# Optimization experiments

Measured on AMD Instinct MI355X. Metric: run time of the kernel, lower is better.

## Reference

```python
import jax, jax.numpy as jnp
import numpy as np

N_NODES = 100000
N_EDGES = 3200000
NUM_FEATURES = 128
DIM = 10
NUM_GRAPHS = 64


def setup_inputs() -> dict:
    key = jax.random.key(0)
    k1, k2, k3, k4, k5, k6, k7 = jax.random.split(key, 7)
    features = jax.random.normal(k1, (N_NODES, NUM_FEATURES), dtype=jnp.float32)
    src = jax.random.randint(k2, (N_EDGES,), 0, N_NODES, dtype=jnp.int64)
    dst = jax.random.randint(k3, (N_EDGES,), 0, N_NODES, dtype=jnp.int64)
    graph_ids = jnp.sort(jax.random.randint(k4, (N_NODES,), 0, NUM_GRAPHS, dtype=jnp.int64))
    # GraphConv weights (no bias), glorot-ish scaling
    W1 = jax.random.normal(k5, (NUM_FEATURES, DIM), dtype=jnp.float32) / np.sqrt(NUM_FEATURES)
    W2 = jax.random.normal(k6, (DIM, DIM), dtype=jnp.float32) / np.sqrt(DIM)
    W3 = jax.random.normal(k7, (DIM, 1), dtype=jnp.float32) / np.sqrt(DIM)
    return {"features": features, "W1": W1, "W2": W2, "W3": W3,
            "src": src, "dst": dst, "graph_ids": graph_ids}


def _sum_aggregate(h, src, dst, n_nodes):
    # message = h[src], reduce-sum at dst (norm='none' GraphConv aggregation)
    return jax.ops.segment_sum(h[src], dst, num_segments=n_nodes)


def reference(features, W1, W2, W3, src, dst, graph_ids):
    n = features.shape[0]
    # conv1: in_feats(128) > out_feats(10) -> weight first, then aggregate
    h = features @ W1                          # [N, DIM]
    h = _sum_aggregate(h, src, dst, n)         # [N, DIM]
    h = jax.nn.relu(h)
    # conv2: in_feats == out_feats -> aggregate first, then weight
    h = _sum_aggregate(h, src, dst, n) @ W2    # [N, DIM]
    # dgl.mean_nodes: per-graph mean pooling over nodes
    sums = jax.ops.segment_sum(h, graph_ids, num_segments=NUM_GRAPHS)           # [G, DIM]
    cnt = jax.ops.segment_sum(jnp.ones((n, 1), h.dtype), graph_ids, num_segments=NUM_GRAPHS)
    pooled = sums / jnp.maximum(cnt, 1.0)      # [G, DIM]
    return jax.nn.sigmoid(pooled @ W3)         # [G, 1]
```

## Files before the change

kernel.cpp:

```cpp
#include <hip/hip_runtime.h>
#include <hip/hip_fp16.h>

#define N_NODES 100000
#define N_EDGES 3200000
#define NUM_FEATURES 128
#define DIM 10
#define NUM_GRAPHS 64

#define BSHIFT 8
#define BSIZE (1 << BSHIFT)
#define NB ((N_NODES + BSIZE - 1) / BSIZE)
#define CHUNKS 2
#define PCHUNKS 4
#define EPB 12500
#define PLACE_BLOCKS 256
#define GEMM_BLOCKS 6250
#define BOUND_BLOCKS 196
#define TILE (BSIZE * DIM)
#define CAP 4608
#define CAPB 16384
#define NCHUNK (NB * CHUNKS)
#define NCHUNK2 (NB * PCHUNKS)
#define ACC_STRIDE 11

__global__ __launch_bounds__(512) void k_front(const float* __restrict__ feat,
                                               const float* __restrict__ W1,
                                               __half* __restrict__ h1,
                                               const int* __restrict__ gids,
                                               int* __restrict__ bound,
                                               const int* __restrict__ src,
                                               const int* __restrict__ dst,
                                               int* __restrict__ cnt,
                                               int* __restrict__ pk) {
    __shared__ int hd[NB];
    __shared__ int cb[NB];

    if (blockIdx.x < PLACE_BLOCKS) {
        int base0 = blockIdx.x * EPB;
        for (int t = threadIdx.x; t < NB; t += 512) hd[t] = 0;
        __syncthreads();

        {
            int i = threadIdx.x;
            for (; i + 1536 < EPB; i += 2048) {
                int d0 = dst[base0 + i],        d1 = dst[base0 + i + 512];
                int d2 = dst[base0 + i + 1024], d3 = dst[base0 + i + 1536];
                atomicAdd(&hd[d0 >> BSHIFT], 1);
                atomicAdd(&hd[d1 >> BSHIFT], 1);
                atomicAdd(&hd[d2 >> BSHIFT], 1);
                atomicAdd(&hd[d3 >> BSHIFT], 1);
            }
            for (; i < EPB; i += 512) {
                int d = dst[base0 + i];
                atomicAdd(&hd[d >> BSHIFT], 1);
            }
        }
        __syncthreads();

        for (int t = threadIdx.x; t < NB; t += 512) {
            int c = hd[t];
            int o = c ? atomicAdd(&cnt[t], c) : 0;
            cb[t] = t * CAPB + o;
        }
        __syncthreads();

        {
            int i = threadIdx.x;
            for (; i + 1536 < EPB; i += 2048) {
                int d0 = dst[base0 + i],        d1 = dst[base0 + i + 512];
                int d2 = dst[base0 + i + 1024], d3 = dst[base0 + i + 1536];
                int s0 = src[base0 + i],        s1 = src[base0 + i + 512];
                int s2 = src[base0 + i + 1024], s3 = src[base0 + i + 1536];
                int q0 = atomicAdd(&cb[d0 >> BSHIFT], 1);
                int q1 = atomicAdd(&cb[d1 >> BSHIFT], 1);
                int q2 = atomicAdd(&cb[d2 >> BSHIFT], 1);
                int q3 = atomicAdd(&cb[d3 >> BSHIFT], 1);
                if (q0 < ((d0 >> BSHIFT) + 1) * CAPB) pk[q0] = ((d0 & (BSIZE - 1)) << 17) | s0;
                if (q1 < ((d1 >> BSHIFT) + 1) * CAPB) pk[q1] = ((d1 & (BSIZE - 1)) << 17) | s1;
                if (q2 < ((d2 >> BSHIFT) + 1) * CAPB) pk[q2] = ((d2 & (BSIZE - 1)) << 17) | s2;
                if (q3 < ((d3 >> BSHIFT) + 1) * CAPB) pk[q3] = ((d3 & (BSIZE - 1)) << 17) | s3;
            }
            for (; i < EPB; i += 512) {
                int d = dst[base0 + i];
                int s = src[base0 + i];
                int q = atomicAdd(&cb[d >> BSHIFT], 1);
                if (q < ((d >> BSHIFT) + 1) * CAPB) pk[q] = ((d & (BSIZE - 1)) << 17) | s;
            }
        }
        return;
    }

    int bb = blockIdx.x - PLACE_BLOCKS;

    int nb2 = bb * 512 + threadIdx.x;
    if (bb < BOUND_BLOCKS && nb2 < N_NODES) {
        int g  = gids[nb2];
        int gp = nb2 ? gids[nb2 - 1] : -1;
        for (int v = gp + 1; v <= g; ++v) bound[v] = nb2;
        if (nb2 == N_NODES - 1)
            for (int v = g + 1; v <= NUM_GRAPHS; ++v) bound[v] = N_NODES;
    }

    int gid  = bb * 512 + threadIdx.x;
    int node = gid >> 5;
    int lane = gid & 31;
    if (node >= N_NODES) return;

    float w[4][DIM];
#pragma unroll
    for (int j = 0; j < 4; ++j)
#pragma unroll
        for (int k = 0; k < DIM; ++k)
            w[j][k] = W1[(lane * 4 + j) * DIM + k];

    const float4 f = *reinterpret_cast<const float4*>(feat + (size_t)node * NUM_FEATURES + lane * 4);
    float fv[4] = {f.x, f.y, f.z, f.w};

    float acc[DIM];
#pragma unroll
    for (int k = 0; k < DIM; ++k) acc[k] = 0.f;
#pragma unroll
    for (int j = 0; j < 4; ++j)
#pragma unroll
        for (int k = 0; k < DIM; ++k)
            acc[k] += fv[j] * w[j][k];

#pragma unroll
    for (int off = 16; off > 0; off >>= 1)
#pragma unroll
        for (int k = 0; k < DIM; ++k)
            acc[k] += __shfl_xor(acc[k], off);

    if (lane == 0) {
        __half2* o = (__half2*)h1;
#pragma unroll
        for (int j = 0; j < 5; ++j)
            o[(size_t)node * 5 + j] = __floats2half2_rn(acc[2 * j], acc[2 * j + 1]);
    }
}

__global__ __launch_bounds__(512) void k_spmm1(const __half* __restrict__ h,
                                               const int* __restrict__ cnt,
                                               const int* __restrict__ pk,
                                               float* __restrict__ part) {
    __shared__ int eh[CAP];
    __shared__ int srt[CAP];
    __shared__ int hist[BSIZE];
    __shared__ int cur[BSIZE];

    int b     = blockIdx.x / CHUNKS;
    int chunk = blockIdx.x % CHUNKS;
    int s0  = b * CAPB;
    int len = cnt[b];
    int c0  = s0 + (len * chunk) / CHUNKS;
    int c1  = s0 + (len * (chunk + 1)) / CHUNKS;
    int n   = c1 - c0;
    int nc  = min(n, CAP);

    for (int t = threadIdx.x; t < BSIZE; t += 512) hist[t] = 0;
    __syncthreads();

    {
        int i = threadIdx.x;
        for (; i + 1536 < nc; i += 2048) {
            int p0 = pk[c0 + i],        p1 = pk[c0 + i + 512];
            int p2 = pk[c0 + i + 1024], p3 = pk[c0 + i + 1536];
            eh[i] = p0; eh[i + 512] = p1; eh[i + 1024] = p2; eh[i + 1536] = p3;
            atomicAdd(&hist[p0 >> 17], 1);
            atomicAdd(&hist[p1 >> 17], 1);
            atomicAdd(&hist[p2 >> 17], 1);
            atomicAdd(&hist[p3 >> 17], 1);
        }
        for (; i < nc; i += 512) {
            int p = pk[c0 + i];
            eh[i] = p;
            atomicAdd(&hist[p >> 17], 1);
        }
    }
    __syncthreads();

    if (threadIdx.x < 64) {
        int l = threadIdx.x;
        int carry = 0;
#pragma unroll
        for (int j = 0; j < 4; ++j) {
            int x = hist[j * 64 + l];
            int v = x;
#pragma unroll
            for (int off = 1; off < 64; off <<= 1) {
                int t2 = __shfl_up(v, off);
                if (l >= off) v += t2;
            }
            cur[j * 64 + l] = carry + v - x;
            carry += __shfl(v, 63);
        }
    }
    __syncthreads();

    for (int i = threadIdx.x; i < nc; i += 512) {
        int p = eh[i];
        int pos = atomicAdd(&cur[p >> 17], 1);
        srt[pos] = p;
    }
    __syncthreads();

    int wave = threadIdx.x >> 6;
    int lane = threadIdx.x & 63;
    int slot = lane / 5;
    int l    = lane - slot * 5;
    float* pb = part + (size_t)blockIdx.x * TILE;
    const __half2* h2 = (const __half2*)h;

    if (slot < 12) {
        int g = wave * 12 + slot;
        for (int loc = g; loc < BSIZE; loc += 96) {
            int e0 = loc ? cur[loc - 1] : 0;
            int e1 = cur[loc];
            float ax0 = 0.f, ay0 = 0.f, ax1 = 0.f, ay1 = 0.f;
            float ax2 = 0.f, ay2 = 0.f, ax3 = 0.f, ay3 = 0.f;
            int e = e0;
            for (; e + 7 < e1; e += 8) {
                float2 v0 = __half22float2(h2[(size_t)(srt[e]     & 0x1FFFF) * 5 + l]);
                float2 v1 = __half22float2(h2[(size_t)(srt[e + 1] & 0x1FFFF) * 5 + l]);
                float2 v2 = __half22float2(h2[(size_t)(srt[e + 2] & 0x1FFFF) * 5 + l]);
                float2 v3 = __half22float2(h2[(size_t)(srt[e + 3] & 0x1FFFF) * 5 + l]);
                float2 v4 = __half22float2(h2[(size_t)(srt[e + 4] & 0x1FFFF) * 5 + l]);
                float2 v5 = __half22float2(h2[(size_t)(srt[e + 5] & 0x1FFFF) * 5 + l]);
                float2 v6 = __half22float2(h2[(size_t)(srt[e + 6] & 0x1FFFF) * 5 + l]);
                float2 v7 = __half22float2(h2[(size_t)(srt[e + 7] & 0x1FFFF) * 5 + l]);
                ax0 += v0.x + v4.x; ay0 += v0.y + v4.y;
                ax1 += v1.x + v5.x; ay1 += v1.y + v5.y;
                ax2 += v2.x + v6.x; ay2 += v2.y + v6.y;
                ax3 += v3.x + v7.x; ay3 += v3.y + v7.y;
            }
            for (; e < e1; ++e) {
                float2 v = __half22float2(h2[(size_t)(srt[e] & 0x1FFFF) * 5 + l]);
                ax0 += v.x; ay0 += v.y;
            }
            pb[loc * DIM + 2 * l]     = (ax0 + ax1) + (ax2 + ax3);
            pb[loc * DIM + 2 * l + 1] = (ay0 + ay1) + (ay2 + ay3);
        }
    }
    __syncthreads();

    for (int i = CAP + threadIdx.x; i < n; i += 512) {
        int p = pk[c0 + i];
        int loc = p >> 17, s = p & 0x1FFFF;
#pragma unroll
        for (int j = 0; j < 5; ++j) {
            float2 v = __half22float2(h2[(size_t)s * 5 + j]);
            atomicAdd(&pb[loc * DIM + 2 * j], v.x);
            atomicAdd(&pb[loc * DIM + 2 * j + 1], v.y);
        }
    }
}

__global__ __launch_bounds__(256) void k_merge_relu(const float* __restrict__ part,
                                                    __half* __restrict__ r) {
    int b     = blockIdx.x;
    int nbase = b << BSHIFT;
    const float* p0 = part + (size_t)(b * CHUNKS) * TILE;
    __half2* r2 = (__half2*)r;
    for (int t = threadIdx.x; t < TILE / 2; t += 256) {
        float sx = 0.f, sy = 0.f;
#pragma unroll
        for (int c = 0; c < CHUNKS; ++c) {
            float2 v = ((const float2*)(p0 + (size_t)c * TILE))[t];
            sx += v.x; sy += v.y;
        }
        int ebase = nbase * DIM + 2 * t;
        if (ebase < N_NODES * DIM)
            r2[(size_t)nbase * 5 + t] = __floats2half2_rn(fmaxf(sx, 0.f), fmaxf(sy, 0.f));
    }
}

__global__ __launch_bounds__(512) void k_pass2(const __half* __restrict__ r,
                                               const int* __restrict__ cnt,
                                               const int* __restrict__ pk,
                                               const int* __restrict__ bound,
                                               float* __restrict__ sums) {
    __shared__ float acc[NUM_GRAPHS * ACC_STRIDE];

    int b     = blockIdx.x / PCHUNKS;
    int chunk = blockIdx.x % PCHUNKS;
    int nbase = b << BSHIFT;
    int nlast = min(nbase + BSIZE - 1, N_NODES - 1);

    int glo = 0, ghx = NUM_GRAPHS - 1;
#pragma unroll
    for (int it = 0; it < 6; ++it) {
        int mid = (glo + ghx + 1) >> 1;
        if (bound[mid] <= nbase) glo = mid; else ghx = mid - 1;
    }
    int lo2 = 0, hi2 = NUM_GRAPHS - 1;
#pragma unroll
    for (int it = 0; it < 6; ++it) {
        int mid = (lo2 + hi2 + 1) >> 1;
        if (bound[mid] <= nlast) lo2 = mid; else hi2 = mid - 1;
    }
    int ghi  = lo2;
    int span = ghi - glo;

    for (int t = threadIdx.x; t < (span + 1) * DIM; t += 512)
        acc[(glo + t / DIM) * ACC_STRIDE + t % DIM] = 0.f;
    __syncthreads();

    int s0  = b * CAPB;
    int len = cnt[b];
    int c0  = s0 + (len * chunk) / PCHUNKS;
    int c1  = s0 + (len * (chunk + 1)) / PCHUNKS;

    int wave = threadIdx.x >> 6;
    int lane = threadIdx.x & 63;
    int slot = lane / 5;
    int l    = lane - slot * 5;
    const __half2* r2 = (const __half2*)r;

    if (slot < 12) {
        const int STR = 96;
        int q = wave * 12 + slot;
        int e = c0 + q;
        if (span <= 1) {
            int gA  = glo;
            int gB  = (span == 1) ? glo + 1 : glo;
            int cut = (span == 1) ? (bound[glo + 1] - nbase) : BSIZE;
            float axA = 0.f, ayA = 0.f, axB = 0.f, ayB = 0.f;
            for (; e + 7 * STR < c1; e += 8 * STR) {
                int p[8];
#pragma unroll
                for (int u = 0; u < 8; ++u) p[u] = pk[e + u * STR];
                float2 v[8];
#pragma unroll
                for (int u = 0; u < 8; ++u)
                    v[u] = __half22float2(r2[(size_t)(p[u] & 0x1FFFF) * 5 + l]);
#pragma unroll
                for (int u = 0; u < 8; ++u) {
                    bool a = (p[u] >> 17) < cut;
                    axA += a ? v[u].x : 0.f;  ayA += a ? v[u].y : 0.f;
                    axB += a ? 0.f : v[u].x;  ayB += a ? 0.f : v[u].y;
                }
            }
            for (; e < c1; e += STR) {
                int p = pk[e];
                float2 v = __half22float2(r2[(size_t)(p & 0x1FFFF) * 5 + l]);
                bool a = (p >> 17) < cut;
                axA += a ? v.x : 0.f;  ayA += a ? v.y : 0.f;
                axB += a ? 0.f : v.x;  ayB += a ? 0.f : v.y;
            }
            atomicAdd(&acc[gA * ACC_STRIDE + 2 * l], axA);
            atomicAdd(&acc[gA * ACC_STRIDE + 2 * l + 1], ayA);
            if (span == 1) {
                atomicAdd(&acc[gB * ACC_STRIDE + 2 * l], axB);
                atomicAdd(&acc[gB * ACC_STRIDE + 2 * l + 1], ayB);
            }
        } else {
            for (; e < c1; e += STR) {
                int p   = pk[e];
                int loc = p >> 17;
                float2 v = __half22float2(r2[(size_t)(p & 0x1FFFF) * 5 + l]);
                int g = glo;
                for (int gg = glo + 1; gg <= ghi; ++gg)
                    g += (loc >= bound[gg] - nbase) ? 1 : 0;
                atomicAdd(&acc[g * ACC_STRIDE + 2 * l], v.x);
                atomicAdd(&acc[g * ACC_STRIDE + 2 * l + 1], v.y);
            }
        }
    }
    __syncthreads();

    for (int t = threadIdx.x; t < (span + 1) * DIM; t += 512) {
        int g = glo + t / DIM;
        float v = acc[g * ACC_STRIDE + t % DIM];
        if (v != 0.f) atomicAdd(&sums[g * DIM + t % DIM], v);
    }
}

__global__ void k_final(const float* __restrict__ sums, const int* __restrict__ bound,
                        const float* __restrict__ W2, const float* __restrict__ W3,
                        float* __restrict__ out) {
    int g = threadIdx.x;
    if (g >= NUM_GRAPHS) return;
    float c = fmaxf((float)(bound[g + 1] - bound[g]), 1.f);
    float p[DIM];
#pragma unroll
    for (int k = 0; k < DIM; ++k) p[k] = sums[g * DIM + k] / c;
    float z = 0.f;
#pragma unroll
    for (int j = 0; j < DIM; ++j) {
        float t = 0.f;
#pragma unroll
        for (int k = 0; k < DIM; ++k) t += p[k] * W2[k * DIM + j];
        z += t * W3[j];
    }
    out[g] = 1.f / (1.f + expf(-z));
}

extern "C" void kernel_launch(void* const* d_in, const int* in_sizes, int n_in,
                              void* d_out, int out_size, void* d_ws, size_t ws_size,
                              hipStream_t stream) {
    const float* feat = (const float*)d_in[0];
    const float* W1   = (const float*)d_in[1];
    const float* W2   = (const float*)d_in[2];
    const float* W3   = (const float*)d_in[3];
    const int*   src  = (const int*)d_in[4];
    const int*   dst  = (const int*)d_in[5];
    const int*   gids = (const int*)d_in[6];
    float*       out  = (float*)d_out;

    char* ws = (char*)d_ws;
    __half* h1    = (__half*)(ws);
    int*    pk    = (int*)(ws + 2000000);
    __half* r     = (__half*)(ws + 27624576);
    float*  part  = (float*)(ws + 29624576);
    int*    cnt   = (int*)(ws + 37632256);
    float*  sums  = (float*)(ws + 37633824);
    int*    bound = (int*)(ws + 37636384);

    hipMemsetAsync(ws + 37632256, 0, 4128, stream);

    k_front<<<PLACE_BLOCKS + GEMM_BLOCKS, 512, 0, stream>>>(feat, W1, h1, gids, bound,
                                                            src, dst, cnt, pk);
    k_spmm1     <<<NCHUNK, 512, 0, stream>>>(h1, cnt, pk, part);
    k_merge_relu<<<NB, 256, 0, stream>>>(part, r);
    k_pass2     <<<NCHUNK2, 512, 0, stream>>>(r, cnt, pk, bound, sums);

    k_final<<<1, 64, 0, stream>>>(sums, bound, W2, W3, out);
}
```

Before: 215.5 us.

## Fuse merge-relu and final into last-block epilogues, DPP reduce, more place blocks

Removes the separate merge/relu and final kernels by having the last-arriving chunk block (tracked by an atomic counter) do the merge+ReLU, and the last pass2 block compute the pooled output. It also replaces the shuffle reduction in the GEMM with DPP row-rotate adds, drops the shared staging buffer in spmm1 by rereading pk from global memory, and doubles the number of placement blocks. Together these cut launch overhead and shared memory use, at the cost of extra global reads and serialized tail work in the elected blocks.

New measurement: 373.3 us. +73.2%, slower.

```diff
diff --git a/kernel.cpp b/kernel.cpp
--- a/kernel.cpp
+++ b/kernel.cpp
@@ -12,8 +12,8 @@
 #define NB ((N_NODES + BSIZE - 1) / BSIZE)
 #define CHUNKS 2
 #define PCHUNKS 4
-#define EPB 12500
-#define PLACE_BLOCKS 256
+#define EPB 6250
+#define PLACE_BLOCKS 512
 #define GEMM_BLOCKS 6250
 #define BOUND_BLOCKS 196
 #define TILE (BSIZE * DIM)
@@ -22,6 +22,10 @@
 #define NCHUNK (NB * CHUNKS)
 #define NCHUNK2 (NB * PCHUNKS)
 #define ACC_STRIDE 11
+
+#define DPP_ROR_ADD(v, n)                                                        \
+    (v) += __int_as_float(__builtin_amdgcn_update_dpp(                           \
+        0, __float_as_int(v), 0x120 | (n), 0xF, 0xF, false))
 
 __global__ __launch_bounds__(512) void k_front(const float* __restrict__ feat,
                                                const float* __restrict__ W1,
@@ -126,10 +130,14 @@
             acc[k] += fv[j] * w[j][k];
 
 #pragma unroll
-    for (int off = 16; off > 0; off >>= 1)
-#pragma unroll
-        for (int k = 0; k < DIM; ++k)
-            acc[k] += __shfl_xor(acc[k], off);
+    for (int k = 0; k < DIM; ++k) {
+        float v = acc[k];
+        DPP_ROR_ADD(v, 1);
+        DPP_ROR_ADD(v, 2);
+        DPP_ROR_ADD(v, 4);
+        DPP_ROR_ADD(v, 8);
+        acc[k] = v + __shfl_xor(v, 16);
+    }
 
     if (lane == 0) {
         __half2* o = (__half2*)h1;
@@ -142,11 +150,13 @@
 __global__ __launch_bounds__(512) void k_spmm1(const __half* __restrict__ h,
                                                const int* __restrict__ cnt,
                                                const int* __restrict__ pk,
-                                               float* __restrict__ part) {
-    __shared__ int eh[CAP];
+                                               float* __restrict__ part,
+                                               int* __restrict__ done,
+                                               __half* __restrict__ r) {
     __shared__ int srt[CAP];
     __shared__ int hist[BSIZE];
     __shared__ int cur[BSIZE];
+    __shared__ int elect;
 
     int b     = blockIdx.x / CHUNKS;
     int chunk = blockIdx.x % CHUNKS;
@@ -165,17 +175,13 @@
         for (; i + 1536 < nc; i += 2048) {
             int p0 = pk[c0 + i],        p1 = pk[c0 + i + 512];
             int p2 = pk[c0 + i + 1024], p3 = pk[c0 + i + 1536];
-            eh[i] = p0; eh[i + 512] = p1; eh[i + 1024] = p2; eh[i + 1536] = p3;
             atomicAdd(&hist[p0 >> 17], 1);
             atomicAdd(&hist[p1 >> 17], 1);
             atomicAdd(&hist[p2 >> 17], 1);
             atomicAdd(&hist[p3 >> 17], 1);
         }
-        for (; i < nc; i += 512) {
-            int p = pk[c0 + i];
-            eh[i] = p;
-            atomicAdd(&hist[p >> 17], 1);
-        }
+        for (; i < nc; i += 512)
+            atomicAdd(&hist[pk[c0 + i] >> 17], 1);
     }
     __syncthreads();
 
@@ -197,10 +203,20 @@
     }
     __syncthreads();
 
-    for (int i = threadIdx.x; i < nc; i += 512) {
-        int p = eh[i];
-        int pos = atomicAdd(&cur[p >> 17], 1);
-        srt[pos] = p;
+    {
+        int i = threadIdx.x;
+        for (; i + 1536 < nc; i += 2048) {
+            int p0 = pk[c0 + i],        p1 = pk[c0 + i + 512];
+            int p2 = pk[c0 + i + 1024], p3 = pk[c0 + i + 1536];
+            srt[atomicAdd(&cur[p0 >> 17], 1)] = p0;
+            srt[atomicAdd(&cur[p1 >> 17], 1)] = p1;
+            srt[atomicAdd(&cur[p2 >> 17], 1)] = p2;
+            srt[atomicAdd(&cur[p3 >> 17], 1)] = p3;
+        }
+        for (; i < nc; i += 512) {
+            int p = pk[c0 + i];
+            srt[atomicAdd(&cur[p >> 17], 1)] = p;
+        }
     }
     __syncthreads();
 
@@ -253,24 +269,29 @@
             atomicAdd(&pb[loc * DIM + 2 * j + 1], v.y);
         }
     }
-}
-
-__global__ __launch_bounds__(256) void k_merge_relu(const float* __restrict__ part,
-                                                    __half* __restrict__ r) {
-    int b     = blockIdx.x;
-    int nbase = b << BSHIFT;
-    const float* p0 = part + (size_t)(b * CHUNKS) * TILE;
-    __half2* r2 = (__half2*)r;
-    for (int t = threadIdx.x; t < TILE / 2; t += 256) {
-        float sx = 0.f, sy = 0.f;
-#pragma unroll
-        for (int c = 0; c < CHUNKS; ++c) {
-            float2 v = ((const float2*)(p0 + (size_t)c * TILE))[t];
-            sx += v.x; sy += v.y;
-        }
-        int ebase = nbase * DIM + 2 * t;
-        if (ebase < N_NODES * DIM)
-            r2[(size_t)nbase * 5 + t] = __floats2half2_rn(fmaxf(sx, 0.f), fmaxf(sy, 0.f));
+    __syncthreads();
+
+    if (threadIdx.x == 0) {
+        __threadfence();
+        elect = (atomicAdd(&done[b], 1) == CHUNKS - 1);
+    }
+    __syncthreads();
+    if (elect) {
+        __threadfence();
+        int nbase = b << BSHIFT;
+        const float* p0 = part + (size_t)(b * CHUNKS) * TILE;
+        __half2* r2 = (__half2*)r;
+        for (int t = threadIdx.x; t < TILE / 2; t += 512) {
+            float sx = 0.f, sy = 0.f;
+#pragma unroll
+            for (int c = 0; c < CHUNKS; ++c) {
+                const float* pp = p0 + (size_t)c * TILE + 2 * t;
+                sx += __hip_atomic_load(pp,     __ATOMIC_RELAXED, __HIP_MEMORY_SCOPE_AGENT);
+                sy += __hip_atomic_load(pp + 1, __ATOMIC_RELAXED, __HIP_MEMORY_SCOPE_AGENT);
+            }
+            if (nbase * DIM + 2 * t < N_NODES * DIM)
+                r2[(size_t)nbase * 5 + t] = __floats2half2_rn(fmaxf(sx, 0.f), fmaxf(sy, 0.f));
+        }
     }
 }
 
@@ -278,8 +299,13 @@
                                                const int* __restrict__ cnt,
                                                const int* __restrict__ pk,
                                                const int* __restrict__ bound,
-                                               float* __restrict__ sums) {
+                                               float* __restrict__ sums,
+                                               int* __restrict__ done2,
+                                               const float* __restrict__ W2,
+                                               const float* __restrict__ W3,
+                                               float* __restrict__ out) {
     __shared__ float acc[NUM_GRAPHS * ACC_STRIDE];
+    __shared__ int elect2;
 
     int b     = blockIdx.x / PCHUNKS;
     int chunk = blockIdx.x % PCHUNKS;
@@ -373,26 +399,32 @@
         float v = acc[g * ACC_STRIDE + t % DIM];
         if (v != 0.f) atomicAdd(&sums[g * DIM + t % DIM], v);
     }
-}
-
-__global__ void k_final(const float* __restrict__ sums, const int* __restrict__ bound,
-                        const float* __restrict__ W2, const float* __restrict__ W3,
-                        float* __restrict__ out) {
-    int g = threadIdx.x;
-    if (g >= NUM_GRAPHS) return;
-    float c = fmaxf((float)(bound[g + 1] - bound[g]), 1.f);
-    float p[DIM];
-#pragma unroll
-    for (int k = 0; k < DIM; ++k) p[k] = sums[g * DIM + k] / c;
-    float z = 0.f;
-#pragma unroll
-    for (int j = 0; j < DIM; ++j) {
-        float t = 0.f;
-#pragma unroll
-        for (int k = 0; k < DIM; ++k) t += p[k] * W2[k * DIM + j];
-        z += t * W3[j];
-    }
-    out[g] = 1.f / (1.f + expf(-z));
+    __syncthreads();
+
+    if (threadIdx.x == 0) {
+        __threadfence();
+        elect2 = (atomicAdd(done2, 1) == NCHUNK2 - 1);
+    }
+    __syncthreads();
+    if (elect2 && threadIdx.x < NUM_GRAPHS) {
+        __threadfence();
+        int g = threadIdx.x;
+        float c = fmaxf((float)(bound[g + 1] - bound[g]), 1.f);
+        float p[DIM];
+#pragma unroll
+        for (int k = 0; k < DIM; ++k)
+            p[k] = __hip_atomic_load(&sums[g * DIM + k], __ATOMIC_RELAXED,
+                                     __HIP_MEMORY_SCOPE_AGENT) / c;
+        float z = 0.f;
+#pragma unroll
+        for (int j = 0; j < DIM; ++j) {
+            float t = 0.f;
+#pragma unroll
+            for (int k = 0; k < DIM; ++k) t += p[k] * W2[k * DIM + j];
+            z += t * W3[j];
+        }
+        out[g] = 1.f / (1.f + expf(-z));
+    }
 }
 
 extern "C" void kernel_launch(void* const* d_in, const int* in_sizes, int n_in,
@@ -413,16 +445,15 @@
     __half* r     = (__half*)(ws + 27624576);
     float*  part  = (float*)(ws + 29624576);
     int*    cnt   = (int*)(ws + 37632256);
-    float*  sums  = (float*)(ws + 37633824);
-    int*    bound = (int*)(ws + 37636384);
-
-    hipMemsetAsync(ws + 37632256, 0, 4128, stream);
+    int*    done  = (int*)(ws + 37633820);
+    int*    done2 = (int*)(ws + 37635384);
+    float*  sums  = (float*)(ws + 37635388);
+    int*    bound = (int*)(ws + 37637948);
+
+    hipMemsetAsync(ws + 37632256, 0, 5692, stream);
 
     k_front<<<PLACE_BLOCKS + GEMM_BLOCKS, 512, 0, stream>>>(feat, W1, h1, gids, bound,
                                                             src, dst, cnt, pk);
-    k_spmm1     <<<NCHUNK, 512, 0, stream>>>(h1, cnt, pk, part);
-    k_merge_relu<<<NB, 256, 0, stream>>>(part, r);
-    k_pass2     <<<NCHUNK2, 512, 0, stream>>>(r, cnt, pk, bound, sums);
-
-    k_final<<<1, 64, 0, stream>>>(sums, bound, W2, W3, out);
+    k_spmm1<<<NCHUNK, 512, 0, stream>>>(h1, cnt, pk, part, done, r);
+    k_pass2<<<NCHUNK2, 512, 0, stream>>>(r, cnt, pk, bound, sums, done2, W2, W3, out);
 }
```
